# Optimization experiments

Measured on AMD Instinct MI355X. Metric: run time of the kernel, lower is better.

The kernel has to match this reference:

```python
import jax, jax.numpy as jnp
import numpy as np

DROP_PROB = 0.5

def setup_inputs() -> dict:
    key = jax.random.key(0)
    k1, k2 = jax.random.split(key)
    N, D = 16384, 4096
    inputs = jax.random.normal(k1, (N, D), dtype=jnp.float32)
    noise = jax.random.uniform(k2, (N, D), dtype=jnp.float32)
    return {"inputs": inputs, "noise": noise}

def reference(inputs, noise):
    # SparseDropout: bernoulli(1-p) mask on nonzero entries, scaled by 1/(1-p).
    # Zeros stay zero under any mask, so this equals plain elementwise dropout.
    keep = (noise >= DROP_PROB).astype(inputs.dtype)
    scale = jnp.asarray(1.0 / (1.0 - DROP_PROB), dtype=inputs.dtype)
    return inputs * keep * scale
```

## Files before the change

kernel.cpp:

```cpp
#include <hip/hip_runtime.h>
#include <hip/hip_bf16.h>

#define DROP_PROB 0.5f
#define SCALE 2.0f

__global__ __launch_bounds__(256) void SparseDropout_kernel(
    const float4* __restrict__ in,
    const float4* __restrict__ noise,
    float4* __restrict__ out,
    int n4)
{
    int i = blockIdx.x * blockDim.x + threadIdx.x;
    if (i < n4) {
        float4 x = in[i];
        float4 nz = noise[i];
        float4 r;
        r.x = (nz.x >= DROP_PROB) ? x.x * SCALE : 0.0f;
        r.y = (nz.y >= DROP_PROB) ? x.y * SCALE : 0.0f;
        r.z = (nz.z >= DROP_PROB) ? x.z * SCALE : 0.0f;
        r.w = (nz.w >= DROP_PROB) ? x.w * SCALE : 0.0f;
        out[i] = r;
    }
}

extern "C" void kernel_launch(void* const* d_in, const int* in_sizes, int n_in,
                              void* d_out, int out_size, void* d_ws, size_t ws_size,
                              hipStream_t stream) {
    const float4* in    = (const float4*)d_in[0];
    const float4* noise = (const float4*)d_in[1];
    float4* out         = (float4*)d_out;

    int n  = out_size;
    int n4 = n / 4;
    int block = 256;
    int grid = (n4 + block - 1) / block;

    SparseDropout_kernel<<<grid, block, 0, stream>>>(in, noise, out, n4);
}
```

Baseline: 565.6 us.

## Use grid-stride loop with 4x unrolled loads and nontemporal stores

Replaces the one-element-per-thread launch with a capped grid of 2048 blocks. Each thread walks a grid-stride loop, issuing four float4 loads from each input before computing and storing. Outputs are written with nontemporal stores to avoid polluting cache with write-only data. The aim is more bytes in flight per thread and less launch and scheduling overhead, at the risk of lower occupancy-driven parallelism from the capped grid.

```diff
diff --git a/kernel.cpp b/kernel.cpp
--- a/kernel.cpp
+++ b/kernel.cpp
@@ -1,8 +1,22 @@
 #include <hip/hip_runtime.h>
-#include <hip/hip_bf16.h>
 
 #define DROP_PROB 0.5f
 #define SCALE 2.0f
+
+typedef float v4f __attribute__((ext_vector_type(4)));
+
+__device__ __forceinline__ float4 drop4(float4 x, float4 z) {
+    float4 r;
+    r.x = (z.x >= DROP_PROB) ? x.x * SCALE : 0.0f;
+    r.y = (z.y >= DROP_PROB) ? x.y * SCALE : 0.0f;
+    r.z = (z.z >= DROP_PROB) ? x.z * SCALE : 0.0f;
+    r.w = (z.w >= DROP_PROB) ? x.w * SCALE : 0.0f;
+    return r;
+}
+
+__device__ __forceinline__ void nt_store4(float4 v, float4* p) {
+    __builtin_nontemporal_store(*(const v4f*)&v, (v4f*)p);
+}
 
 __global__ __launch_bounds__(256) void SparseDropout_kernel(
     const float4* __restrict__ in,
@@ -10,16 +24,34 @@
     float4* __restrict__ out,
     int n4)
 {
+    const int stride = gridDim.x * blockDim.x;
     int i = blockIdx.x * blockDim.x + threadIdx.x;
-    if (i < n4) {
+
+    for (; i + 3 * stride < n4; i += 4 * stride) {
+        const int i0 = i;
+        const int i1 = i + stride;
+        const int i2 = i + 2 * stride;
+        const int i3 = i + 3 * stride;
+
+        float4 x0 = in[i0];
+        float4 x1 = in[i1];
+        float4 x2 = in[i2];
+        float4 x3 = in[i3];
+        float4 z0 = noise[i0];
+        float4 z1 = noise[i1];
+        float4 z2 = noise[i2];
+        float4 z3 = noise[i3];
+
+        nt_store4(drop4(x0, z0), &out[i0]);
+        nt_store4(drop4(x1, z1), &out[i1]);
+        nt_store4(drop4(x2, z2), &out[i2]);
+        nt_store4(drop4(x3, z3), &out[i3]);
+    }
+
+    for (; i < n4; i += stride) {
         float4 x = in[i];
-        float4 nz = noise[i];
-        float4 r;
-        r.x = (nz.x >= DROP_PROB) ? x.x * SCALE : 0.0f;
-        r.y = (nz.y >= DROP_PROB) ? x.y * SCALE : 0.0f;
-        r.z = (nz.z >= DROP_PROB) ? x.z * SCALE : 0.0f;
-        r.w = (nz.w >= DROP_PROB) ? x.w * SCALE : 0.0f;
-        out[i] = r;
+        float4 z = noise[i];
+        nt_store4(drop4(x, z), &out[i]);
     }
 }
 
@@ -32,8 +64,11 @@
 
     int n  = out_size;
     int n4 = n / 4;
+
     int block = 256;
+    int max_blocks = 2048;
     int grid = (n4 + block - 1) / block;
+    if (grid > max_blocks) grid = max_blocks;
 
     SparseDropout_kernel<<<grid, block, 0, stream>>>(in, noise, out, n4);
 }
```

After: 628.0 us. 11.0% more time.
